# Kernel tuning notes

Hardware: AMD Instinct MI355X
Metric: run time of the kernel (lower is better)

Reference implementation:

```python
import jax, jax.numpy as jnp
import numpy as np

N = 200000          # active voxels
C = 128             # channels (in == out, required by final elementwise multiply)
GRID = (256, 256, 64)
EPS = 1e-5


def setup_inputs() -> dict:
    rng = np.random.default_rng(0)
    total = GRID[0] * GRID[1] * GRID[2]
    lin = rng.choice(total, size=N, replace=False)
    coords = np.stack(np.unravel_index(lin, GRID), axis=1).astype(np.int64)  # [N,3]
    # dense voxel -> row lookup table; sentinel N means 'no active voxel here'
    lut = np.full(total, N, dtype=np.int32)
    lut[lin] = np.arange(N, dtype=np.int32)
    nb = np.full((3, 2, N), N, dtype=np.int32)  # [axis, {prev,next}, N]
    hi = np.array(GRID) - 1
    for a in range(3):
        for s, off in enumerate((-1, 1)):
            c = coords.copy()
            c[:, a] += off
            valid = (c[:, a] >= 0) & (c[:, a] <= hi[a])
            cc = np.clip(c, 0, hi)
            lin_n = np.ravel_multi_index(tuple(cc.T), GRID)
            nb[a, s] = np.where(valid, lut[lin_n], N)
    kf, kw, kg, kb = jax.random.split(jax.random.key(0), 4)
    features = jax.random.normal(kf, (N, C), jnp.float32)
    W = jax.random.normal(kw, (3, 3, C, C), jnp.float32) * (1.0 / np.sqrt(3.0 * C))
    gamma = 1.0 + 0.1 * jax.random.normal(kg, (3, C), jnp.float32)
    beta = 0.1 * jax.random.normal(kb, (3, C), jnp.float32)
    return {"features": features, "nb_idx": jnp.asarray(nb), "W": W,
            "gamma": gamma, "beta": beta}


def reference(features, nb_idx, W, gamma, beta):
    # zero pad row: gathering sentinel index N yields a zero contribution
    xp = jnp.concatenate([features, jnp.zeros((1, C), features.dtype)], axis=0)
    acc = jnp.zeros_like(features)
    for a in range(3):  # three 1D decomposition axes (3x1x1, 1x3x1, 1x1x3)
        prev = xp[nb_idx[a, 0]]                      # [N,C]
        nxt = xp[nb_idx[a, 1]]                       # [N,C]
        out = prev @ W[a, 0] + features @ W[a, 1] + nxt @ W[a, 2]
        # BatchNorm1d (training-mode batch stats, biased variance)
        mu = out.mean(axis=0)
        var = out.var(axis=0)
        out = (out - mu) * jax.lax.rsqrt(var + EPS) * gamma[a] + beta[a]
        acc = acc + jax.nn.sigmoid(out)
    return acc * features
```

## Files before the change

kernel.cpp:

```cpp
#include <hip/hip_runtime.h>
#include <hip/hip_bf16.h>

#define NVOX 200000
#define CCH  128
#define KTOT 384
#define EPS_BN 1e-5f
#define PB   625
#define TPB  5
#define NTILE 3125

typedef __bf16 bf16x8 __attribute__((ext_vector_type(8)));
typedef __bf16 bf16x4 __attribute__((ext_vector_type(4)));
typedef float  floatx4 __attribute__((ext_vector_type(4)));

#define XBF_OFF    0ull
#define XBF_BYTES  ((size_t)(NVOX + 1) * CCH * 2)
#define WT_OFF     (XBF_OFF + XBF_BYTES)
#define WT_BYTES   ((size_t)3 * CCH * KTOT * 2)
#define OUTB_OFF   (WT_OFF + WT_BYTES)
#define OUTB_BYTES ((size_t)3 * NVOX * CCH * 2)
#define STATS_OFF  (OUTB_OFF + OUTB_BYTES)
#define STATS_BYTES ((size_t)3 * 2 * CCH * 4)

__global__ void k_prep(const float* __restrict__ xf, __bf16* __restrict__ xbf,
                       const float* __restrict__ W, __bf16* __restrict__ wt,
                       float* __restrict__ stats) {
    int idx = blockIdx.x * blockDim.x + threadIdx.x;
    const int XC = (NVOX + 1) * 16;
    if (idx < XC) {
        float v[8];
        if (idx < NVOX * 16) {
            const float4* p = (const float4*)xf + (size_t)idx * 2;
            float4 f0 = p[0], f1 = p[1];
            v[0] = f0.x; v[1] = f0.y; v[2] = f0.z; v[3] = f0.w;
            v[4] = f1.x; v[5] = f1.y; v[6] = f1.z; v[7] = f1.w;
        } else {
            #pragma unroll
            for (int j = 0; j < 8; ++j) v[j] = 0.0f;
        }
        bf16x8 o;
        #pragma unroll
        for (int j = 0; j < 8; ++j) o[j] = (__bf16)v[j];
        *((bf16x8*)xbf + idx) = o;
    } else if (idx < XC + 3 * CCH * KTOT) {
        int j = idx - XC;
        int k = j % KTOT; int rem = j / KTOT;
        int c = rem % CCH;  int a = rem / CCH;
        int s = k >> 7, k0 = k & 127;
        wt[j] = (__bf16)W[(((size_t)(a * 3 + s) * CCH) + k0) * CCH + c];
    } else if (idx < XC + 3 * CCH * KTOT + 768) {
        stats[idx - XC - 3 * CCH * KTOT] = 0.0f;
    }
}

#define LDS_PAD 2560
__launch_bounds__(256, 2)
__global__ void k_gemm(const __bf16* __restrict__ xbf, const __bf16* __restrict__ wt,
                       const int* __restrict__ nb, __bf16* __restrict__ outb,
                       float* __restrict__ stats) {
    __shared__ __align__(16) __bf16 smemA[64 * 384 + LDS_PAD];
    __shared__ int s_pn[2][128];

    const int a    = blockIdx.y;
    const int tid  = threadIdx.x;
    const int w    = tid >> 6;
    const int lane = tid & 63;
    const int q    = lane >> 4;
    const int ln   = lane & 15;
    const int e    = ln & 7;

    if (tid == 0) smemA[64 * 384 + (blockIdx.x & (LDS_PAD - 1))] = (__bf16)0.0f;

    const __bf16* wbase = wt + (size_t)a * CCH * KTOT;
    bf16x8 B0[12], B1[12];
    #pragma unroll
    for (int ks = 0; ks < 12; ++ks) {
        B0[ks] = *(const bf16x8*)(wbase + (size_t)(w * 32 + ln) * KTOT + ks * 32 + q * 8);
        B1[ks] = *(const bf16x8*)(wbase + (size_t)(w * 32 + 16 + ln) * KTOT + ks * 32 + q * 8);
    }

    float s0 = 0.f, ss0 = 0.f, s1 = 0.f, ss1 = 0.f;

    int r_pn = 0;
    if (tid < 128) {
        const size_t nbase = (size_t)(a * 2 + (tid >> 6)) * NVOX + (tid & 63);
        r_pn = nb[nbase + blockIdx.x * 64];
        s_pn[0][tid] = r_pn;
        r_pn = nb[nbase + (blockIdx.x + PB) * 64];
    }
    __syncthreads();

    for (int ti = 0; ti < TPB; ++ti) {
        const int tIdx = blockIdx.x + ti * PB;
        const int row0 = tIdx * 64;
        const int buf  = ti & 1;

        #pragma unroll
        for (int it = 0; it < 12; ++it) {
            int p    = it * 256 + tid;
            int r    = p / 48;
            int spos = p - r * 48;
            int slog = spos ^ (r & 7);
            int src  = slog >> 4, ch = slog & 15;
            int g    = (src == 1) ? (row0 + r) : s_pn[buf][(src >> 1) * 64 + r];
            const __bf16* gp = xbf + (size_t)g * CCH + ch * 8;
            __builtin_amdgcn_global_load_lds(
                (const __attribute__((address_space(1))) void*)gp,
                (__attribute__((address_space(3))) void*)(&smemA[(it * 256 + w * 64) * 8]),
                16, 0, 0);
        }
        if (ti + 1 < TPB && tid < 128) s_pn[buf ^ 1][tid] = r_pn;
        __syncthreads();

        if (ti + 2 < TPB && tid < 128)
            r_pn = nb[(size_t)(a * 2 + (tid >> 6)) * NVOX
                      + (blockIdx.x + (ti + 2) * PB) * 64 + (tid & 63)];

        floatx4 acc0[4], acc1[4];
        #pragma unroll
        for (int mt = 0; mt < 4; ++mt)
            #pragma unroll
            for (int r = 0; r < 4; ++r) { acc0[mt][r] = 0.0f; acc1[mt][r] = 0.0f; }

        #pragma unroll
        for (int ks = 0; ks < 12; ++ks) {
            #pragma unroll
            for (int mt = 0; mt < 4; ++mt) {
                bf16x8 afr = *(const bf16x8*)(&smemA[(mt * 16 + ln) * 384 + (((ks * 4 + q) ^ e) * 8)]);
                acc0[mt] = __builtin_amdgcn_mfma_f32_16x16x32_bf16(afr, B0[ks], acc0[mt], 0, 0, 0);
                acc1[mt] = __builtin_amdgcn_mfma_f32_16x16x32_bf16(afr, B1[ks], acc1[mt], 0, 0, 0);
            }
        }

        {
            __bf16* ob = outb + ((size_t)(a * NTILE + tIdx)) * 8192 + lane * 4;
            #pragma unroll
            for (int mt = 0; mt < 4; ++mt) {
                bf16x4 v0, v1;
                #pragma unroll
                for (int r = 0; r < 4; ++r) {
                    float f0 = acc0[mt][r]; s0 += f0; ss0 += f0 * f0; v0[r] = (__bf16)f0;
                    float f1 = acc1[mt][r]; s1 += f1; ss1 += f1 * f1; v1[r] = (__bf16)f1;
                }
                *(bf16x4*)(ob + ((w * 2 + 0) * 4 + mt) * 256) = v0;
                *(bf16x4*)(ob + ((w * 2 + 1) * 4 + mt) * 256) = v1;
            }
        }

        __syncthreads();
    }

    s0 += __shfl_xor(s0, 16); ss0 += __shfl_xor(ss0, 16);
    s0 += __shfl_xor(s0, 32); ss0 += __shfl_xor(ss0, 32);
    s1 += __shfl_xor(s1, 16); ss1 += __shfl_xor(ss1, 16);
    s1 += __shfl_xor(s1, 32); ss1 += __shfl_xor(ss1, 32);
    if (lane < 16) {
        int c0 = w * 32 + lane, c1 = w * 32 + 16 + lane;
        atomicAdd(&stats[a * 2 * CCH + c0], s0);
        atomicAdd(&stats[a * 2 * CCH + CCH + c0], ss0);
        atomicAdd(&stats[a * 2 * CCH + c1], s1);
        atomicAdd(&stats[a * 2 * CCH + CCH + c1], ss1);
    }
}

__launch_bounds__(256)
__global__ void k_final(const __bf16* __restrict__ outb, const float* __restrict__ xf,
                        const float* __restrict__ stats, const float* __restrict__ gamma,
                        const float* __restrict__ beta, float* __restrict__ out) {
    __shared__ float lsc[384], lsh[384];
    int tid = threadIdx.x;
    for (int i = tid; i < 384; i += 256) {
        int a = i >> 7, c = i & 127;
        float mu  = stats[a * 256 + c] * (1.0f / NVOX);
        float var = stats[a * 256 + 128 + c] * (1.0f / NVOX) - mu * mu;
        float rs  = rsqrtf(var + EPS_BN);
        float g = gamma[i], b = beta[i];
        lsc[i] = rs * g;
        lsh[i] = b - mu * rs * g;
    }
    __syncthreads();
    const int total = NTILE * 2048;
    for (int c = blockIdx.x * 256 + tid; c < total; c += gridDim.x * 256) {
        int t     = c >> 11;
        int cc    = c & 2047;
        int g     = cc >> 6;
        int lane2 = cc & 63;
        int mt    = g & 3, h = g >> 2;
        int qq    = lane2 >> 4, lnn = lane2 & 15;
        int col   = h * 16 + lnn;
        int row   = t * 64 + mt * 16 + qq * 4;
        float r[4] = {0.f, 0.f, 0.f, 0.f};
        #pragma unroll
        for (int a = 0; a < 3; ++a) {
            bf16x4 o = *(const bf16x4*)(outb + ((size_t)(a * NTILE + t)) * 8192 + g * 256 + lane2 * 4);
            float sc = lsc[a * 128 + col], sh = lsh[a * 128 + col];
            #pragma unroll
            for (int j = 0; j < 4; ++j) {
                float v = (float)o[j] * sc + sh;
                r[j] += __builtin_amdgcn_rcpf(1.0f + __expf(-v));
            }
        }
        #pragma unroll
        for (int j = 0; j < 4; ++j) {
            size_t off = (size_t)(row + j) * CCH + col;
            out[off] = r[j] * xf[off];
        }
    }
}

extern "C" void kernel_launch(void* const* d_in, const int* in_sizes, int n_in,
                              void* d_out, int out_size, void* d_ws, size_t ws_size,
                              hipStream_t stream) {
    const float* xf    = (const float*)d_in[0];
    const int*   nb    = (const int*)  d_in[1];
    const float* W     = (const float*)d_in[2];
    const float* gamma = (const float*)d_in[3];
    const float* beta  = (const float*)d_in[4];
    float* out = (float*)d_out;

    char* ws = (char*)d_ws;
    __bf16* xbf   = (__bf16*)(ws + XBF_OFF);
    __bf16* wt    = (__bf16*)(ws + WT_OFF);
    __bf16* outb  = (__bf16*)(ws + OUTB_OFF);
    float*  stats = (float*)(ws + STATS_OFF);

    const int prep_items = (NVOX + 1) * 16 + 3 * CCH * KTOT + 768;
    k_prep<<<(prep_items + 255) / 256, 256, 0, stream>>>(xf, xbf, W, wt, stats);
    k_gemm<<<dim3(PB, 3), 256, 0, stream>>>(xbf, wt, nb, outb, stats);
    k_final<<<2048, 256, 0, stream>>>(outb, xf, stats, gamma, beta, out);
}
```

Before: 371.7 us.

## Double-buffer 32-row gather tiles in GEMM and coalesce final epilogue via LDS transpose

The GEMM kernel now uses 32-row tiles with two LDS buffers, prefetching the next tile's neighbour gather while MFMAs run on the current one, and drops the trailing barrier. The final kernel now runs one block per 32-row tile and stages sigmoid sums in LDS so features and outputs are read and written as coalesced float4. This targets exposed gather latency and strided epilogue stores. The cost is half the rows per MFMA pass per wave, which raises per-tile overhead and sync count, plus more blocks in the final kernel.

```diff
diff --git a/kernel.cpp b/kernel.cpp
--- a/kernel.cpp
+++ b/kernel.cpp
@@ -5,9 +5,10 @@
 #define CCH  128
 #define KTOT 384
 #define EPS_BN 1e-5f
-#define PB   625
-#define TPB  5
-#define NTILE 3125
+#define PB    625
+#define TROWS 32
+#define TPB   10
+#define NT2   6250
 
 typedef __bf16 bf16x8 __attribute__((ext_vector_type(8)));
 typedef __bf16 bf16x4 __attribute__((ext_vector_type(4)));
@@ -58,8 +59,9 @@
 __global__ void k_gemm(const __bf16* __restrict__ xbf, const __bf16* __restrict__ wt,
                        const int* __restrict__ nb, __bf16* __restrict__ outb,
                        float* __restrict__ stats) {
-    __shared__ __align__(16) __bf16 smemA[64 * 384 + LDS_PAD];
-    __shared__ int s_pn[2][128];
+    __shared__ __align__(16) __bf16 smemA[2][TROWS * 384];
+    __shared__ __bf16 smemPad[LDS_PAD];
+    __shared__ int s_pn[2][64];
 
     const int a    = blockIdx.y;
     const int tid  = threadIdx.x;
@@ -69,7 +71,7 @@
     const int ln   = lane & 15;
     const int e    = ln & 7;
 
-    if (tid == 0) smemA[64 * 384 + (blockIdx.x & (LDS_PAD - 1))] = (__bf16)0.0f;
+    if (tid == 0) smemPad[blockIdx.x & (LDS_PAD - 1)] = (__bf16)0.0f;
 
     const __bf16* wbase = wt + (size_t)a * CCH * KTOT;
     bf16x8 B0[12], B1[12];
@@ -82,72 +84,87 @@
     float s0 = 0.f, ss0 = 0.f, s1 = 0.f, ss1 = 0.f;
 
     int r_pn = 0;
-    if (tid < 128) {
-        const size_t nbase = (size_t)(a * 2 + (tid >> 6)) * NVOX + (tid & 63);
-        r_pn = nb[nbase + blockIdx.x * 64];
+    if (tid < 64) {
+        const size_t nbase = (size_t)(a * 2 + (tid >> 5)) * NVOX + (tid & 31);
+        r_pn = nb[nbase + blockIdx.x * TROWS];
         s_pn[0][tid] = r_pn;
-        r_pn = nb[nbase + (blockIdx.x + PB) * 64];
+        r_pn = nb[nbase + (blockIdx.x + PB) * TROWS];
     }
     __syncthreads();
+    {
+        const int row0 = blockIdx.x * TROWS;
+        #pragma unroll
+        for (int it = 0; it < 6; ++it) {
+            int p    = it * 256 + tid;
+            int r    = p / 48;
+            int seg  = p - r * 48;
+            int slog = seg ^ (r & 7);
+            int src  = slog >> 4, ch = slog & 15;
+            int g    = (src == 1) ? (row0 + r) : s_pn[0][(src >> 1) * 32 + r];
+            __builtin_amdgcn_global_load_lds(
+                (const __attribute__((address_space(1))) void*)(xbf + (size_t)g * CCH + ch * 8),
+                (__attribute__((address_space(3))) void*)(&smemA[0][(it * 256 + w * 64) * 8]),
+                16, 0, 0);
+        }
+    }
 
     for (int ti = 0; ti < TPB; ++ti) {
         const int tIdx = blockIdx.x + ti * PB;
-        const int row0 = tIdx * 64;
         const int buf  = ti & 1;
 
-        #pragma unroll
-        for (int it = 0; it < 12; ++it) {
-            int p    = it * 256 + tid;
-            int r    = p / 48;
-            int spos = p - r * 48;
-            int slog = spos ^ (r & 7);
-            int src  = slog >> 4, ch = slog & 15;
-            int g    = (src == 1) ? (row0 + r) : s_pn[buf][(src >> 1) * 64 + r];
-            const __bf16* gp = xbf + (size_t)g * CCH + ch * 8;
-            __builtin_amdgcn_global_load_lds(
-                (const __attribute__((address_space(1))) void*)gp,
-                (__attribute__((address_space(3))) void*)(&smemA[(it * 256 + w * 64) * 8]),
-                16, 0, 0);
-        }
-        if (ti + 1 < TPB && tid < 128) s_pn[buf ^ 1][tid] = r_pn;
+        if (ti + 1 < TPB && tid < 64) s_pn[buf ^ 1][tid] = r_pn;
         __syncthreads();
 
-        if (ti + 2 < TPB && tid < 128)
-            r_pn = nb[(size_t)(a * 2 + (tid >> 6)) * NVOX
-                      + (blockIdx.x + (ti + 2) * PB) * 64 + (tid & 63)];
-
-        floatx4 acc0[4], acc1[4];
-        #pragma unroll
-        for (int mt = 0; mt < 4; ++mt)
+        if (ti + 1 < TPB) {
+            const int rown = (blockIdx.x + (ti + 1) * PB) * TROWS;
+            #pragma unroll
+            for (int it = 0; it < 6; ++it) {
+                int p    = it * 256 + tid;
+                int r    = p / 48;
+                int seg  = p - r * 48;
+                int slog = seg ^ (r & 7);
+                int src  = slog >> 4, ch = slog & 15;
+                int g    = (src == 1) ? (rown + r) : s_pn[buf ^ 1][(src >> 1) * 32 + r];
+                __builtin_amdgcn_global_load_lds(
+                    (const __attribute__((address_space(1))) void*)(xbf + (size_t)g * CCH + ch * 8),
+                    (__attribute__((address_space(3))) void*)(&smemA[buf ^ 1][(it * 256 + w * 64) * 8]),
+                    16, 0, 0);
+            }
+        }
+        if (ti + 2 < TPB && tid < 64)
+            r_pn = nb[(size_t)(a * 2 + (tid >> 5)) * NVOX
+                      + (blockIdx.x + (ti + 2) * PB) * TROWS + (tid & 31)];
+
+        floatx4 acc0[2], acc1[2];
+        #pragma unroll
+        for (int mt = 0; mt < 2; ++mt)
             #pragma unroll
             for (int r = 0; r < 4; ++r) { acc0[mt][r] = 0.0f; acc1[mt][r] = 0.0f; }
 
         #pragma unroll
         for (int ks = 0; ks < 12; ++ks) {
             #pragma unroll
-            for (int mt = 0; mt < 4; ++mt) {
-                bf16x8 afr = *(const bf16x8*)(&smemA[(mt * 16 + ln) * 384 + (((ks * 4 + q) ^ e) * 8)]);
+            for (int mt = 0; mt < 2; ++mt) {
+                bf16x8 afr = *(const bf16x8*)(&smemA[buf][(mt * 16 + ln) * 384 + (((ks * 4 + q) ^ e) * 8)]);
                 acc0[mt] = __builtin_amdgcn_mfma_f32_16x16x32_bf16(afr, B0[ks], acc0[mt], 0, 0, 0);
                 acc1[mt] = __builtin_amdgcn_mfma_f32_16x16x32_bf16(afr, B1[ks], acc1[mt], 0, 0, 0);
             }
         }
 
         {
-            __bf16* ob = outb + ((size_t)(a * NTILE + tIdx)) * 8192 + lane * 4;
-            #pragma unroll
-            for (int mt = 0; mt < 4; ++mt) {
+            __bf16* ob = outb + ((size_t)(a * NT2 + tIdx)) * 4096 + lane * 4;
+            #pragma unroll
+            for (int mt = 0; mt < 2; ++mt) {
                 bf16x4 v0, v1;
                 #pragma unroll
                 for (int r = 0; r < 4; ++r) {
                     float f0 = acc0[mt][r]; s0 += f0; ss0 += f0 * f0; v0[r] = (__bf16)f0;
                     float f1 = acc1[mt][r]; s1 += f1; ss1 += f1 * f1; v1[r] = (__bf16)f1;
                 }
-                *(bf16x4*)(ob + ((w * 2 + 0) * 4 + mt) * 256) = v0;
-                *(bf16x4*)(ob + ((w * 2 + 1) * 4 + mt) * 256) = v1;
-            }
-        }
-
-        __syncthreads();
+                *(bf16x4*)(ob + ((w * 2 + 0) * 2 + mt) * 256) = v0;
+                *(bf16x4*)(ob + ((w * 2 + 1) * 2 + mt) * 256) = v1;
+            }
+        }
     }
 
     s0 += __shfl_xor(s0, 16); ss0 += __shfl_xor(ss0, 16);
@@ -168,7 +185,8 @@
                         const float* __restrict__ stats, const float* __restrict__ gamma,
                         const float* __restrict__ beta, float* __restrict__ out) {
     __shared__ float lsc[384], lsh[384];
-    int tid = threadIdx.x;
+    __shared__ float tile[TROWS * 132];
+    const int tid = threadIdx.x;
     for (int i = tid; i < 384; i += 256) {
         int a = i >> 7, c = i & 127;
         float mu  = stats[a * 256 + c] * (1.0f / NVOX);
@@ -179,32 +197,51 @@
         lsh[i] = b - mu * rs * g;
     }
     __syncthreads();
-    const int total = NTILE * 2048;
-    for (int c = blockIdx.x * 256 + tid; c < total; c += gridDim.x * 256) {
-        int t     = c >> 11;
-        int cc    = c & 2047;
-        int g     = cc >> 6;
-        int lane2 = cc & 63;
-        int mt    = g & 3, h = g >> 2;
-        int qq    = lane2 >> 4, lnn = lane2 & 15;
-        int col   = h * 16 + lnn;
-        int row   = t * 64 + mt * 16 + qq * 4;
-        float r[4] = {0.f, 0.f, 0.f, 0.f};
-        #pragma unroll
-        for (int a = 0; a < 3; ++a) {
-            bf16x4 o = *(const bf16x4*)(outb + ((size_t)(a * NTILE + t)) * 8192 + g * 256 + lane2 * 4);
+
+    const int t = blockIdx.x;
+
+    float racc[16];
+    #pragma unroll
+    for (int j = 0; j < 16; ++j) racc[j] = 0.0f;
+    #pragma unroll
+    for (int a = 0; a < 3; ++a) {
+        #pragma unroll
+        for (int k = 0; k < 4; ++k) {
+            int cidx = k * 256 + tid;
+            bf16x4 o = *(const bf16x4*)(outb + ((size_t)(a * NT2 + t)) * 4096 + cidx * 4);
+            int g = cidx >> 6, l2 = cidx & 63;
+            int col = (g >> 1) * 16 + (l2 & 15);
             float sc = lsc[a * 128 + col], sh = lsh[a * 128 + col];
             #pragma unroll
             for (int j = 0; j < 4; ++j) {
                 float v = (float)o[j] * sc + sh;
-                r[j] += __builtin_amdgcn_rcpf(1.0f + __expf(-v));
-            }
-        }
-        #pragma unroll
-        for (int j = 0; j < 4; ++j) {
-            size_t off = (size_t)(row + j) * CCH + col;
-            out[off] = r[j] * xf[off];
-        }
+                racc[k * 4 + j] += __builtin_amdgcn_rcpf(1.0f + __expf(-v));
+            }
+        }
+    }
+
+    #pragma unroll
+    for (int k = 0; k < 4; ++k) {
+        int cidx = k * 256 + tid;
+        int g = cidx >> 6, l2 = cidx & 63;
+        int row = (g & 1) * 16 + (l2 >> 4) * 4;
+        int col = (g >> 1) * 16 + (l2 & 15);
+        #pragma unroll
+        for (int j = 0; j < 4; ++j)
+            tile[(row + j) * 132 + col] = racc[k * 4 + j];
+    }
+    __syncthreads();
+
+    #pragma unroll
+    for (int k = 0; k < 4; ++k) {
+        int fc  = k * 256 + tid;
+        int row = fc >> 5, c4 = fc & 31;
+        float4 v = *(float4*)&tile[row * 132 + c4 * 4];
+        size_t f4idx = (size_t)(t * TROWS + row) * 32 + c4;
+        float4 f = ((const float4*)xf)[f4idx];
+        float4 o;
+        o.x = v.x * f.x; o.y = v.y * f.y; o.z = v.z * f.z; o.w = v.w * f.w;
+        ((float4*)out)[f4idx] = o;
     }
 }
 
@@ -227,5 +264,5 @@
     const int prep_items = (NVOX + 1) * 16 + 3 * CCH * KTOT + 768;
     k_prep<<<(prep_items + 255) / 256, 256, 0, stream>>>(xf, xbf, W, wt, stats);
     k_gemm<<<dim3(PB, 3), 256, 0, stream>>>(xbf, wt, nb, outb, stats);
-    k_final<<<2048, 256, 0, stream>>>(outb, xf, stats, gamma, beta, out);
-}
+    k_final<<<NT2, 256, 0, stream>>>(outb, xf, stats, gamma, beta, out);
+}
```

Result: faster. 350.9 us (-5.6%).
